# Kernel tuning notes

Hardware: AMD Instinct MI355X
Metric: run time of the kernel (lower is better)

Reference implementation:

```python
import jax, jax.numpy as jnp
import numpy as np

T, B, D = 2048, 256, 32
H0, H1, O = 64, 64, 35


def _fastgrnn_scan(xs, h0, W, U, bg, bu, zeta, nu):
    """Run FastGRNN recurrence. xs: [T, N, Din], h0: [N, H] -> hiddenStates [T, N, H].
    z = sigmoid(xW + hU + bg); c = tanh(xW + hU + bu);
    h = z*h + (sigmoid(zeta)*(1-z) + sigmoid(nu))*c
    """
    zs = jax.nn.sigmoid(zeta)  # [1,1]
    ns = jax.nn.sigmoid(nu)    # [1,1]
    xW = jnp.einsum('tnd,dh->tnh', xs, W)  # precompute input projections (same math)

    def step(h, xw):
        pre = xw + h @ U
        z = jax.nn.sigmoid(pre + bg)
        c = jnp.tanh(pre + bu)
        h_new = z * h + (zs * (1.0 - z) + ns) * c
        return h_new, h_new

    _, hs = jax.lax.scan(step, h0, xW)
    return hs


def setup_inputs() -> dict:
    key = jax.random.key(0)
    ks = jax.random.split(key, 8)
    x = jax.random.normal(ks[0], (T, B, D), dtype=jnp.float32)
    # FastGRNNCell params, layer 0 (inputDim -> hiddenDim0), full-rank (wRank=uRank=None)
    W0 = 0.1 * jax.random.normal(ks[1], (D, H0), dtype=jnp.float32)
    U0 = 0.1 * jax.random.normal(ks[2], (H0, H0), dtype=jnp.float32)
    bg0 = jnp.ones((1, H0), jnp.float32)
    bu0 = jnp.ones((1, H0), jnp.float32)
    zeta0 = 1.0 * jnp.ones((1, 1), jnp.float32)
    nu0 = -4.0 * jnp.ones((1, 1), jnp.float32)
    # layer 1 (hiddenDim0 -> hiddenDim1)
    W1 = 0.1 * jax.random.normal(ks[3], (H0, H1), dtype=jnp.float32)
    U1 = 0.1 * jax.random.normal(ks[4], (H1, H1), dtype=jnp.float32)
    bg1 = jnp.ones((1, H1), jnp.float32)
    bu1 = jnp.ones((1, H1), jnp.float32)
    zeta1 = 1.0 * jnp.ones((1, 1), jnp.float32)
    nu1 = -4.0 * jnp.ones((1, 1), jnp.float32)
    # output projection
    Wout = jax.random.normal(ks[5], (H1, O), dtype=jnp.float32)
    Bout = jax.random.normal(ks[6], (O,), dtype=jnp.float32)
    return {
        'x': x, 'brickSize': 32,
        'W0': W0, 'U0': U0, 'bg0': bg0, 'bu0': bu0, 'zeta0': zeta0, 'nu0': nu0,
        'W1': W1, 'U1': U1, 'bg1': bg1, 'bu1': bu1, 'zeta1': zeta1, 'nu1': nu1,
        'Wout': Wout, 'Bout': Bout,
    }


def reference(x, brickSize, W0, U0, bg0, bu0, zeta0, nu0,
              W1, U1, bg1, bu1, zeta1, nu1, Wout, Bout):
    t, b, d = x.shape
    numBricks = t // brickSize
    x = x[:numBricks * brickSize]
    # brick: [numBricks, brickSize, B, D] -> [brickSize, numBricks*B, D]
    xb = x.reshape(numBricks, brickSize, b, d)
    xb = jnp.transpose(xb, (1, 0, 2, 3)).reshape(brickSize, numBricks * b, d)
    # layer-0 FastGRNN over the brick time axis
    h0_init = jnp.zeros((numBricks * b, W0.shape[1]), x.dtype)
    hs0 = _fastgrnn_scan(xb, h0_init, W0, U0, bg0, bu0, zeta0, nu0)
    last0 = hs0[-1].reshape(numBricks, b, W0.shape[1])  # [numBricks, B, H0]
    # layer-1 FastGRNN over the brick axis
    h1_init = jnp.zeros((b, W1.shape[1]), x.dtype)
    hs1 = _fastgrnn_scan(last0, h1_init, W1, U1, bg1, bu1, zeta1, nu1)
    out = hs1[-1] @ Wout + Bout  # [B, outputDim]
    return out
```

## Files before the change

### kernel.cpp

```cpp
#include <hip/hip_runtime.h>
#include <hip/hip_bf16.h>


#define NB    64
#define BS    32
#define BATCH 256
#define D0    32
#define H     64
#define OUTD  35

typedef short  bf8   __attribute__((ext_vector_type(8)));
typedef float  f32x4 __attribute__((ext_vector_type(4)));

__device__ __forceinline__ float sigm(float x) {
    return 1.0f / (1.0f + __expf(-x));
}
__device__ __forceinline__ float tanh_safe(float x) {
    float a = fabsf(x);
    float e = __expf(-2.0f * a);
    float m = (1.0f - e) / (1.0f + e);
    return copysignf(m, x);
}
__device__ __forceinline__ short f2bf(float f) {
    __hip_bfloat16 b = __float2bfloat16(f);
    return __builtin_bit_cast(short, b);
}

__global__ __launch_bounds__(1024, 4) void l0_kernel(
    const float* __restrict__ x,
    const float* __restrict__ W,
    const float* __restrict__ U,
    const float* __restrict__ bg,
    const float* __restrict__ bu,
    const float* __restrict__ zeta,
    const float* __restrict__ nu,
    float* __restrict__ last0)
{
    __shared__ unsigned char hb[2][64 * 128];

    const int tid  = threadIdx.x;
    const int lane = tid & 63;
    const int wave = tid >> 6;
    const int wm   = __builtin_amdgcn_readfirstlane(wave >> 2);
    const int wn   = __builtin_amdgcn_readfirstlane(wave & 3);
    const int l15  = lane & 15;
    const int lg   = lane >> 4;

    const int brick     = blockIdx.x >> 2;
    const int batchbase = (blockIdx.x & 3) << 6;

    *reinterpret_cast<float2*>(&hb[0][tid * 8]) = make_float2(0.f, 0.f);

    bf8 Wb, Ub0, Ub1;
    const int ucol = wn * 16 + l15;
#pragma unroll
    for (int j = 0; j < 8; ++j) Wb[j]  = f2bf(W[(8 * lg + j) * H + ucol]);
#pragma unroll
    for (int j = 0; j < 8; ++j) Ub0[j] = f2bf(U[(8 * lg + j) * H + ucol]);
#pragma unroll
    for (int j = 0; j < 8; ++j) Ub1[j] = f2bf(U[(32 + 8 * lg + j) * H + ucol]);

    const float bgc = bg[ucol], buc = bu[ucol];
    const float zs  = sigm(zeta[0]);
    const float ns  = sigm(nu[0]);

    float hc[4] = {0.f, 0.f, 0.f, 0.f};

    const float* xbase = x + ((size_t)(brick * BS) * BATCH + batchbase + wm * 16 + l15) * D0 + 8 * lg;
    const size_t xstep = (size_t)BATCH * D0;

    float4 xa0 = reinterpret_cast<const float4*>(xbase)[0];
    float4 xa1 = reinterpret_cast<const float4*>(xbase)[1];
    float4 xn0 = reinterpret_cast<const float4*>(xbase + xstep)[0];
    float4 xn1 = reinterpret_cast<const float4*>(xbase + xstep)[1];

    __syncthreads();

    int cur = 0;
#pragma unroll 1
    for (int t = 0; t < BS; ++t) {
        float4 p0 = make_float4(0.f, 0.f, 0.f, 0.f), p1 = p0;
        if (t + 2 < BS) {
            p0 = reinterpret_cast<const float4*>(xbase + (size_t)(t + 2) * xstep)[0];
            p1 = reinterpret_cast<const float4*>(xbase + (size_t)(t + 2) * xstep)[1];
        }

        bf8 xa;
        xa[0] = f2bf(xa0.x); xa[1] = f2bf(xa0.y); xa[2] = f2bf(xa0.z); xa[3] = f2bf(xa0.w);
        xa[4] = f2bf(xa1.x); xa[5] = f2bf(xa1.y); xa[6] = f2bf(xa1.z); xa[7] = f2bf(xa1.w);

        f32x4 acc = {0.f, 0.f, 0.f, 0.f};
        acc = __builtin_amdgcn_mfma_f32_16x16x32_bf16(xa, Wb, acc, 0, 0, 0);

        const int srow = wm * 16 + l15;
        const unsigned char* hr = &hb[cur][srow * 128];
        bf8 ha0 = *reinterpret_cast<const bf8*>(hr + ((16 * lg) ^ ((srow & 7) << 4)));
        bf8 ha1 = *reinterpret_cast<const bf8*>(hr + ((64 + 16 * lg) ^ ((srow & 7) << 4)));
        acc = __builtin_amdgcn_mfma_f32_16x16x32_bf16(ha0, Ub0, acc, 0, 0, 0);
        acc = __builtin_amdgcn_mfma_f32_16x16x32_bf16(ha1, Ub1, acc, 0, 0, 0);

#pragma unroll
        for (int r = 0; r < 4; ++r) {
            float pre = acc[r];
            float z = sigm(pre + bgc);
            float c = tanh_safe(pre + buc);
            hc[r] = z * hc[r] + (zs * (1.f - z) + ns) * c;
        }

        {
            unsigned char* wb = &hb[cur ^ 1][0];
#pragma unroll
            for (int r = 0; r < 4; ++r) {
                int s   = wm * 16 + 4 * lg + r;
                int off = s * 128 + ((ucol * 2) ^ ((s & 7) << 4));
                *reinterpret_cast<short*>(wb + off) = f2bf(hc[r]);
            }
        }
        __syncthreads();
        cur ^= 1;
        xa0 = xn0; xa1 = xn1;
        xn0 = p0;  xn1 = p1;
    }

    {
        float* op = last0 + ((size_t)(brick * BATCH + batchbase)) * H;
#pragma unroll
        for (int r = 0; r < 4; ++r) {
            int s = wm * 16 + 4 * lg + r;
            op[(size_t)s * H + ucol] = hc[r];
        }
    }
}

__global__ __launch_bounds__(256, 1) void l1_kernel(
    const float* __restrict__ last0,
    const float* __restrict__ W,
    const float* __restrict__ U,
    const float* __restrict__ bg,
    const float* __restrict__ bu,
    const float* __restrict__ zeta,
    const float* __restrict__ nu,
    const float* __restrict__ Wout,
    const float* __restrict__ Bout,
    float* __restrict__ out)
{
    __shared__ float px[NB][H];
    __shared__ float hbb[H];

    const int lane  = threadIdx.x & 63;
    const int wave  = __builtin_amdgcn_readfirstlane(threadIdx.x >> 6);
    const int batch = blockIdx.x;

    float wc[H];
#pragma unroll
    for (int k = 0; k < H; ++k) wc[k] = W[k * H + lane];

#pragma unroll 1
    for (int t = wave * 16; t < wave * 16 + 16; ++t) {
        const float* ip = last0 + ((size_t)(t * BATCH + batch)) * H;
        float a = 0.f;
#pragma unroll
        for (int k = 0; k < H; ++k) a = fmaf(ip[k], wc[k], a);
        px[t][lane] = a;
    }
    __syncthreads();
    if (wave != 0) return;

    float uc[H];
#pragma unroll
    for (int k = 0; k < H; ++k) uc[k] = U[k * H + lane];

    const float zs  = sigm(zeta[0]);
    const float ns  = sigm(nu[0]);
    const float bgj = bg[lane];
    const float buj = bu[lane];

    float h = 0.f;
    hbb[lane] = 0.f;

#pragma unroll 1
    for (int t = 0; t < NB; ++t) {
        float a = px[t][lane];
#pragma unroll
        for (int q = 0; q < H / 4; ++q) {
            float4 hv = *reinterpret_cast<const float4*>(&hbb[4 * q]);
            a = fmaf(hv.x, uc[4 * q + 0], a);
            a = fmaf(hv.y, uc[4 * q + 1], a);
            a = fmaf(hv.z, uc[4 * q + 2], a);
            a = fmaf(hv.w, uc[4 * q + 3], a);
        }
        float z = sigm(a + bgj);
        float c = tanh_safe(a + buj);
        h = z * h + (zs * (1.f - z) + ns) * c;
        hbb[lane] = h;
    }

    if (lane < OUTD) {
        float o = Bout[lane];
#pragma unroll
        for (int k = 0; k < H; ++k) o = fmaf(hbb[k], Wout[k * OUTD + lane], o);
        out[batch * OUTD + lane] = o;
    }
}

extern "C" void kernel_launch(void* const* d_in, const int* in_sizes, int n_in,
                              void* d_out, int out_size, void* d_ws, size_t ws_size,
                              hipStream_t stream) {
    const float* x    = (const float*)d_in[0];
    const float* W0   = (const float*)d_in[2];
    const float* U0   = (const float*)d_in[3];
    const float* bg0  = (const float*)d_in[4];
    const float* bu0  = (const float*)d_in[5];
    const float* z0   = (const float*)d_in[6];
    const float* n0   = (const float*)d_in[7];
    const float* W1   = (const float*)d_in[8];
    const float* U1   = (const float*)d_in[9];
    const float* bg1  = (const float*)d_in[10];
    const float* bu1  = (const float*)d_in[11];
    const float* z1   = (const float*)d_in[12];
    const float* n1   = (const float*)d_in[13];
    const float* Wout = (const float*)d_in[14];
    const float* Bout = (const float*)d_in[15];
    float* out = (float*)d_out;

    float* last0 = (float*)d_ws;

    l0_kernel<<<256, 1024, 0, stream>>>(x, W0, U0, bg0, bu0, z0, n0, last0);
    l1_kernel<<<BATCH, 256, 0, stream>>>(last0, W1, U1, bg1, bu1, z1, n1, Wout, Bout, out);
}
```

Before: 85.72 us.

## Split layer-0 blocks to 16 rows, use fast reciprocal, split FMA chains

```diff
diff --git a/kernel.cpp b/kernel.cpp
--- a/kernel.cpp
+++ b/kernel.cpp
@@ -12,13 +12,16 @@
 typedef short  bf8   __attribute__((ext_vector_type(8)));
 typedef float  f32x4 __attribute__((ext_vector_type(4)));
 
+__device__ __forceinline__ float rcp_fast(float x) {
+    return __builtin_amdgcn_rcpf(x);
+}
 __device__ __forceinline__ float sigm(float x) {
-    return 1.0f / (1.0f + __expf(-x));
+    return rcp_fast(1.0f + __expf(-x));
 }
 __device__ __forceinline__ float tanh_safe(float x) {
     float a = fabsf(x);
     float e = __expf(-2.0f * a);
-    float m = (1.0f - e) / (1.0f + e);
+    float m = (1.0f - e) * rcp_fast(1.0f + e);
     return copysignf(m, x);
 }
 __device__ __forceinline__ short f2bf(float f) {
@@ -26,7 +29,7 @@
     return __builtin_bit_cast(short, b);
 }
 
-__global__ __launch_bounds__(1024, 4) void l0_kernel(
+__global__ __launch_bounds__(256, 4) void l0_kernel(
     const float* __restrict__ x,
     const float* __restrict__ W,
     const float* __restrict__ U,
@@ -36,18 +39,16 @@
     const float* __restrict__ nu,
     float* __restrict__ last0)
 {
-    __shared__ unsigned char hb[2][64 * 128];
+    __shared__ unsigned char hb[2][16 * 128];
 
     const int tid  = threadIdx.x;
     const int lane = tid & 63;
-    const int wave = tid >> 6;
-    const int wm   = __builtin_amdgcn_readfirstlane(wave >> 2);
-    const int wn   = __builtin_amdgcn_readfirstlane(wave & 3);
+    const int wn   = __builtin_amdgcn_readfirstlane(tid >> 6);
     const int l15  = lane & 15;
     const int lg   = lane >> 4;
 
-    const int brick     = blockIdx.x >> 2;
-    const int batchbase = (blockIdx.x & 3) << 6;
+    const int brick     = blockIdx.x >> 4;
+    const int batchbase = (blockIdx.x & 15) << 4;
 
     *reinterpret_cast<float2*>(&hb[0][tid * 8]) = make_float2(0.f, 0.f);
 
@@ -66,7 +67,7 @@
 
     float hc[4] = {0.f, 0.f, 0.f, 0.f};
 
-    const float* xbase = x + ((size_t)(brick * BS) * BATCH + batchbase + wm * 16 + l15) * D0 + 8 * lg;
+    const float* xbase = x + ((size_t)(brick * BS) * BATCH + batchbase + l15) * D0 + 8 * lg;
     const size_t xstep = (size_t)BATCH * D0;
 
     float4 xa0 = reinterpret_cast<const float4*>(xbase)[0];
@@ -79,11 +80,9 @@
     int cur = 0;
 #pragma unroll 1
     for (int t = 0; t < BS; ++t) {
-        float4 p0 = make_float4(0.f, 0.f, 0.f, 0.f), p1 = p0;
-        if (t + 2 < BS) {
-            p0 = reinterpret_cast<const float4*>(xbase + (size_t)(t + 2) * xstep)[0];
-            p1 = reinterpret_cast<const float4*>(xbase + (size_t)(t + 2) * xstep)[1];
-        }
+        const int tp = (t + 2 < BS) ? (t + 2) : (BS - 1);
+        float4 p0 = reinterpret_cast<const float4*>(xbase + (size_t)tp * xstep)[0];
+        float4 p1 = reinterpret_cast<const float4*>(xbase + (size_t)tp * xstep)[1];
 
         bf8 xa;
         xa[0] = f2bf(xa0.x); xa[1] = f2bf(xa0.y); xa[2] = f2bf(xa0.z); xa[3] = f2bf(xa0.w);
@@ -92,10 +91,10 @@
         f32x4 acc = {0.f, 0.f, 0.f, 0.f};
         acc = __builtin_amdgcn_mfma_f32_16x16x32_bf16(xa, Wb, acc, 0, 0, 0);
 
-        const int srow = wm * 16 + l15;
-        const unsigned char* hr = &hb[cur][srow * 128];
-        bf8 ha0 = *reinterpret_cast<const bf8*>(hr + ((16 * lg) ^ ((srow & 7) << 4)));
-        bf8 ha1 = *reinterpret_cast<const bf8*>(hr + ((64 + 16 * lg) ^ ((srow & 7) << 4)));
+        const unsigned char* hr = &hb[cur][l15 * 128];
+        const int swz = (l15 & 7) << 4;
+        bf8 ha0 = *reinterpret_cast<const bf8*>(hr + ((16 * lg) ^ swz));
+        bf8 ha1 = *reinterpret_cast<const bf8*>(hr + ((64 + 16 * lg) ^ swz));
         acc = __builtin_amdgcn_mfma_f32_16x16x32_bf16(ha0, Ub0, acc, 0, 0, 0);
         acc = __builtin_amdgcn_mfma_f32_16x16x32_bf16(ha1, Ub1, acc, 0, 0, 0);
 
@@ -111,7 +110,7 @@
             unsigned char* wb = &hb[cur ^ 1][0];
 #pragma unroll
             for (int r = 0; r < 4; ++r) {
-                int s   = wm * 16 + 4 * lg + r;
+                int s   = 4 * lg + r;
                 int off = s * 128 + ((ucol * 2) ^ ((s & 7) << 4));
                 *reinterpret_cast<short*>(wb + off) = f2bf(hc[r]);
             }
@@ -126,7 +125,7 @@
         float* op = last0 + ((size_t)(brick * BATCH + batchbase)) * H;
 #pragma unroll
         for (int r = 0; r < 4; ++r) {
-            int s = wm * 16 + 4 * lg + r;
+            int s = 4 * lg + r;
             op[(size_t)s * H + ucol] = hc[r];
         }
     }
@@ -158,10 +157,15 @@
 #pragma unroll 1
     for (int t = wave * 16; t < wave * 16 + 16; ++t) {
         const float* ip = last0 + ((size_t)(t * BATCH + batch)) * H;
-        float a = 0.f;
-#pragma unroll
-        for (int k = 0; k < H; ++k) a = fmaf(ip[k], wc[k], a);
-        px[t][lane] = a;
+        float a0 = 0.f, a1 = 0.f, a2 = 0.f, a3 = 0.f;
+#pragma unroll
+        for (int q = 0; q < H / 4; ++q) {
+            a0 = fmaf(ip[4 * q + 0], wc[4 * q + 0], a0);
+            a1 = fmaf(ip[4 * q + 1], wc[4 * q + 1], a1);
+            a2 = fmaf(ip[4 * q + 2], wc[4 * q + 2], a2);
+            a3 = fmaf(ip[4 * q + 3], wc[4 * q + 3], a3);
+        }
+        px[t][lane] = (a0 + a1) + (a2 + a3);
     }
     __syncthreads();
     if (wave != 0) return;
@@ -180,15 +184,16 @@
 
 #pragma unroll 1
     for (int t = 0; t < NB; ++t) {
-        float a = px[t][lane];
+        float a0 = px[t][lane], a1 = 0.f, a2 = 0.f, a3 = 0.f;
 #pragma unroll
         for (int q = 0; q < H / 4; ++q) {
             float4 hv = *reinterpret_cast<const float4*>(&hbb[4 * q]);
-            a = fmaf(hv.x, uc[4 * q + 0], a);
-            a = fmaf(hv.y, uc[4 * q + 1], a);
-            a = fmaf(hv.z, uc[4 * q + 2], a);
-            a = fmaf(hv.w, uc[4 * q + 3], a);
-        }
+            a0 = fmaf(hv.x, uc[4 * q + 0], a0);
+            a1 = fmaf(hv.y, uc[4 * q + 1], a1);
+            a2 = fmaf(hv.z, uc[4 * q + 2], a2);
+            a3 = fmaf(hv.w, uc[4 * q + 3], a3);
+        }
+        float a = (a0 + a1) + (a2 + a3);
         float z = sigm(a + bgj);
         float c = tanh_safe(a + buj);
         h = z * h + (zs * (1.f - z) + ns) * c;
@@ -225,6 +230,6 @@
 
     float* last0 = (float*)d_ws;
 
-    l0_kernel<<<256, 1024, 0, stream>>>(x, W0, U0, bg0, bu0, z0, n0, last0);
+    l0_kernel<<<1024, 256, 0, stream>>>(x, W0, U0, bg0, bu0, z0, n0, last0);
     l1_kernel<<<BATCH, 256, 0, stream>>>(last0, W1, U1, bg1, bu1, z1, n1, Wout, Bout, out);
 }
```

Measured after the change: 72.95 us. -14.9%, faster.
